# Kernel optimization log

Measured on AMD Instinct MI355X. Metric: run time of the kernel, lower is better.

Reference implementation:

```python
import jax, jax.numpy as jnp
import numpy as np

N = 100000          # num nodes
E = 500000          # num edges
D_IN = 32           # in_channels
D_OUT = 32          # out_channels (== in_channels, required by per-edge bmm)
NUM_REL = 16


def setup_inputs() -> dict:
    key = jax.random.key(0)
    k1, k2, k3, k4, k5, k6 = jax.random.split(key, 6)
    x = jax.random.normal(k1, (N, D_IN), dtype=jnp.float32)
    edge_index = jax.random.randint(k2, (2, E), 0, N)
    edge_type = jax.random.randint(k3, (E,), 0, NUM_REL)
    # Linear(in, out, bias=False): weight stored [in, out] here (x @ W)
    W = jax.random.normal(k4, (D_IN, D_OUT), dtype=jnp.float32) / np.sqrt(D_IN)
    # nn.Embedding(num_relations, in*out)
    rel_emb = jax.random.normal(k5, (NUM_REL, D_IN * D_OUT), dtype=jnp.float32)
    # attention vector, xavier-uniform-ish
    lim = float(1.414 * np.sqrt(6.0 / (D_OUT + 1)))
    attention = jax.random.uniform(k6, (D_OUT, 1), minval=-lim, maxval=lim, dtype=jnp.float32)
    return {"x": x, "edge_index": edge_index, "edge_type": edge_type,
            "W": W, "rel_emb": rel_emb, "attention": attention}


def reference(x, edge_index, edge_type, W, rel_emb, attention):
    # x = self.weight(x)
    h = x @ W                                            # [N, D_OUT]
    # per-edge relation transform: rel_trans [E, D_IN, D_OUT]
    rel = rel_emb[edge_type].reshape(-1, D_IN, D_OUT)    # [E, D_IN, D_OUT]
    src = edge_index[0]
    dst = edge_index[1]
    # messages = bmm(x[src], rel_trans) -> per-edge matvec
    msg = jnp.einsum('ei,eio->eo', h[src], rel)          # [E, D_OUT]
    # scatter-add into destination node buckets
    out = jax.ops.segment_sum(msg, dst, num_segments=N)  # [N, D_OUT]
    # global attention softmax over all nodes (dim=0)
    scores = (out @ attention)[:, 0]                     # [N]
    weights = jax.nn.softmax(scores, axis=0)             # [N]
    # dropout omitted (eval mode / deterministic reference)
    out = jax.nn.relu(out * weights[:, None])
    return out
```

## Files before the change

kernel.cpp:

```cpp
#include <hip/hip_runtime.h>

static constexpr int NN  = 100000;
static constexpr int NE  = 500000;
static constexpr int D   = 32;
static constexpr int NR  = 16;
static constexpr int HB  = 256;
static constexpr int ES  = (NE + HB - 1) / HB;
static constexpr int CAP = 33000;
static constexpr int NY  = 128;

__global__ __launch_bounds__(256) void k_prep(const int* __restrict__ ei,
                                              const int* __restrict__ et,
                                              const float* __restrict__ W,
                                              const float* __restrict__ rel,
                                              float* __restrict__ wr,
                                              int* __restrict__ cursor,
                                              int2* __restrict__ rec,
                                              float* __restrict__ outz) {
    __shared__ int lh[NR], lcur[NR];
    if (threadIdx.x < NR) lh[threadIdx.x] = 0;
    __syncthreads();

    {
        float4* oz = reinterpret_cast<float4*>(outz);
        const int total4 = NN * D / 4;
        for (int i = blockIdx.x * 256 + threadIdx.x; i < total4; i += HB * 256)
            oz[i] = make_float4(0.f, 0.f, 0.f, 0.f);
    }

    if (blockIdx.x < NR) {
        const int t = blockIdx.x;
        for (int idx = threadIdx.x; idx < D * D; idx += 256) {
            const int i = idx >> 5;
            const int o = idx & 31;
            const float* Wr = W + i * D;
            const float* Rr = rel + t * (D * D) + o;
            float s = 0.f;
            #pragma unroll
            for (int j = 0; j < D; ++j)
                s = fmaf(Wr[j], Rr[j * D], s);
            wr[t * (D * D) + idx] = s;
        }
    }

    const int beg = blockIdx.x * ES, end = min(beg + ES, NE);
    for (int e = beg + (int)threadIdx.x; e < end; e += 256)
        atomicAdd(&lh[et[e]], 1);
    __syncthreads();
    if (threadIdx.x < NR)
        lcur[threadIdx.x] = (lh[threadIdx.x] > 0)
                          ? atomicAdd(&cursor[threadIdx.x], lh[threadIdx.x])
                          : 0;
    __syncthreads();
    for (int e = beg + (int)threadIdx.x; e < end; e += 256) {
        const int t = et[e];
        const int rank = min(atomicAdd(&lcur[t], 1), CAP - 1);
        rec[t * CAP + rank] = make_int2(ei[e], ei[NE + e]);
    }
}

__global__ __launch_bounds__(256) void k_edge(const float* __restrict__ x,
                                              const int2* __restrict__ rec,
                                              const int* __restrict__ cnt,
                                              const float* __restrict__ wr,
                                              float* __restrict__ acc) {
    const int t    = blockIdx.x & (NR - 1);
    const int c    = blockIdx.x >> 4;
    const int lane = threadIdx.x & 63;
    const int wv   = threadIdx.x >> 6;
    const int half = lane >> 5;
    const int o    = lane & 31;
    const int r8   = lane >> 3;
    const int q8   = lane & 7;

    __shared__ float sx[4][2][8][36];
    __shared__ int   sd[4][2][8];

    float Rc[32];
    {
        const float* __restrict__ Rt = wr + t * 1024;
        #pragma unroll
        for (int i = 0; i < 32; ++i) Rc[i] = Rt[i * 32 + o];
    }

    const int beg  = t * CAP;
    const int cntt = min(cnt[t], CAP);
    if (cntt <= 0) return;
    const int elast = beg + cntt - 1;
    const int ngrp  = (cntt + 7) >> 3;
    const int nw    = NY * 4;
    const int wid   = c * 4 + wv;
    if (wid >= ngrp) return;

    int2 rr0 = rec[min(beg + wid * 8 + r8, elast)];
    int2 rr1 = rec[min(beg + (wid + nw) * 8 + r8, elast)];
    int2 rr2 = rec[min(beg + (wid + 2 * nw) * 8 + r8, elast)];
    float4 xv0 = reinterpret_cast<const float4*>(x + (size_t)rr0.x * D)[q8];

    int buf = 0;
    for (int grp = wid; grp < ngrp; grp += nw) {
        *reinterpret_cast<float4*>(&sx[wv][buf][r8][q8 * 4]) = xv0;
        if (q8 == 0) sd[wv][buf][r8] = rr0.y;

        float4 xv1 = reinterpret_cast<const float4*>(x + (size_t)rr1.x * D)[q8];
        int2 rr3 = rec[min(beg + (grp + 3 * nw) * 8 + r8, elast)];

        __asm__ volatile("s_waitcnt lgkmcnt(0)" ::: "memory");

        const int lbase = grp * 8;
        #pragma unroll
        for (int jj = 0; jj < 4; ++jj) {
            const int row = jj * 2 + half;
            const float* rp = &sx[wv][buf][row][0];
            float p = 0.f;
            #pragma unroll
            for (int q = 0; q < 8; ++q) {
                const float4 v = *reinterpret_cast<const float4*>(rp + q * 4);
                p = fmaf(v.x, Rc[4*q+0], p);
                p = fmaf(v.y, Rc[4*q+1], p);
                p = fmaf(v.z, Rc[4*q+2], p);
                p = fmaf(v.w, Rc[4*q+3], p);
            }
            if (lbase + row < cntt) {
                const int dd = sd[wv][buf][row];
                atomicAdd(acc + (size_t)dd * D + o, p);
            }
        }
        rr0 = rr1; rr1 = rr2; rr2 = rr3; xv0 = xv1;
        buf ^= 1;
    }
}

__global__ __launch_bounds__(256) void k_score(const float* __restrict__ acc,
                                               const float* __restrict__ att,
                                               float* __restrict__ scores,
                                               float* __restrict__ pmax,
                                               float* __restrict__ psum) {
    __shared__ float sA[D];
    __shared__ float shm[4], shs[4];
    if (threadIdx.x < D) sA[threadIdx.x] = att[threadIdx.x];
    __syncthreads();
    const int n = blockIdx.x * 256 + threadIdx.x;
    float s = -3.4e38f;
    if (n < NN) {
        const float4* av = reinterpret_cast<const float4*>(acc + (size_t)n * D);
        float v0 = 0.f;
        #pragma unroll
        for (int k = 0; k < 8; ++k) {
            float4 v = av[k];
            v0 += v.x * sA[4*k+0] + v.y * sA[4*k+1] + v.z * sA[4*k+2] + v.w * sA[4*k+3];
        }
        scores[n] = v0;
        s = v0;
    }
    float m = s;
    #pragma unroll
    for (int offt = 32; offt > 0; offt >>= 1)
        m = fmaxf(m, __shfl_down(m, offt, 64));
    if ((threadIdx.x & 63) == 0) shm[threadIdx.x >> 6] = m;
    __syncthreads();
    const float bm = fmaxf(fmaxf(shm[0], shm[1]), fmaxf(shm[2], shm[3]));
    float e = (n < NN) ? expf(s - bm) : 0.f;
    #pragma unroll
    for (int offt = 32; offt > 0; offt >>= 1)
        e += __shfl_down(e, offt, 64);
    if ((threadIdx.x & 63) == 0) shs[threadIdx.x >> 6] = e;
    __syncthreads();
    if (threadIdx.x == 0) {
        pmax[blockIdx.x] = bm;
        psum[blockIdx.x] = shs[0] + shs[1] + shs[2] + shs[3];
    }
}

__global__ __launch_bounds__(256) void k_final(float* __restrict__ out,
                                               const float* __restrict__ scores,
                                               const float* __restrict__ pmax,
                                               const float* __restrict__ psum,
                                               int nb) {
    __shared__ float shm[4], shs[4];
    const int tid = threadIdx.x;
    float m = -3.4e38f, s = 0.f;
    for (int i = tid; i < nb; i += 256) {
        const float mi = pmax[i], si = psum[i];
        const float M = fmaxf(m, mi);
        s = s * expf(m - M) + si * expf(mi - M);
        m = M;
    }
    #pragma unroll
    for (int offt = 32; offt > 0; offt >>= 1) {
        const float mo = __shfl_down(m, offt, 64);
        const float so = __shfl_down(s, offt, 64);
        const float M = fmaxf(m, mo);
        s = s * expf(m - M) + so * expf(mo - M);
        m = M;
    }
    if ((tid & 63) == 0) { shm[tid >> 6] = m; shs[tid >> 6] = s; }
    __syncthreads();
    float M = shm[0], S = shs[0];
    #pragma unroll
    for (int w = 1; w < 4; ++w) {
        const float Mn = fmaxf(M, shm[w]);
        S = S * expf(M - Mn) + shs[w] * expf(shm[w] - Mn);
        M = Mn;
    }
    const int idx = blockIdx.x * 256 + tid;
    const int n = idx >> 3;
    const float w = expf(scores[n] - M) / S;
    float4* p = reinterpret_cast<float4*>(out);
    float4 v = p[idx];
    v.x = fmaxf(v.x * w, 0.f);
    v.y = fmaxf(v.y * w, 0.f);
    v.z = fmaxf(v.z * w, 0.f);
    v.w = fmaxf(v.w * w, 0.f);
    p[idx] = v;
}

extern "C" void kernel_launch(void* const* d_in, const int* in_sizes, int n_in,
                              void* d_out, int out_size, void* d_ws, size_t ws_size,
                              hipStream_t stream) {
    const float* x   = (const float*)d_in[0];
    const int*   ei  = (const int*)  d_in[1];
    const int*   et  = (const int*)  d_in[2];
    const float* W   = (const float*)d_in[3];
    const float* rel = (const float*)d_in[4];
    const float* att = (const float*)d_in[5];
    float* out = (float*)d_out;

    float* wr     = (float*)d_ws;
    int2*  rec    = (int2*)(wr + NR * D * D);
    int*   cursor = (int*)(rec + NR * CAP);
    float* pmax   = (float*)(cursor + NR);
    float* psum   = pmax + 512;
    float* scores = (float*)rec;

    hipMemsetAsync(cursor, 0, NR * sizeof(int), stream);

    k_prep<<<HB, 256, 0, stream>>>(ei, et, W, rel, wr, cursor, rec, out);
    k_edge<<<NR * NY, 256, 0, stream>>>(x, rec, cursor, wr, out);

    const int nb_n = (NN + 255) / 256;
    k_score<<<nb_n, 256, 0, stream>>>(out, att, scores, pmax, psum);
    k_final<<<(NN * (D / 4)) / 256, 256, 0, stream>>>(out, scores, pmax, psum, nb_n);
}
```

Before: 95.89 us.

## Accumulate messages in fp16 half2 atomics and fuse attention score into edge kernel

Switches the scatter-add accumulator from fp32 to fp16 using packed half2 atomics, halving the number and size of atomic ops per edge. It also computes the attention score per edge with a cross-lane shuffle reduction and accumulates it with one fp32 atomic per edge. This removes the score kernel's full read of the accumulator. The final kernel converts fp16 back to fp32 output. This risks accuracy loss from fp16 accumulation and adds shuffle work in the edge loop.

Result: faster. 88.47 us, median of 2 (-7.7%).

```diff
diff --git a/kernel.cpp b/kernel.cpp
--- a/kernel.cpp
+++ b/kernel.cpp
@@ -1,4 +1,5 @@
 #include <hip/hip_runtime.h>
+#include <hip/hip_fp16.h>
 
 static constexpr int NN  = 100000;
 static constexpr int NE  = 500000;
@@ -16,16 +17,15 @@
                                               float* __restrict__ wr,
                                               int* __restrict__ cursor,
                                               int2* __restrict__ rec,
-                                              float* __restrict__ outz) {
+                                              float4* __restrict__ zbase) {
     __shared__ int lh[NR], lcur[NR];
     if (threadIdx.x < NR) lh[threadIdx.x] = 0;
     __syncthreads();
 
     {
-        float4* oz = reinterpret_cast<float4*>(outz);
-        const int total4 = NN * D / 4;
+        const int total4 = (NN * D * 2 + NN * 4) / 16;
         for (int i = blockIdx.x * 256 + threadIdx.x; i < total4; i += HB * 256)
-            oz[i] = make_float4(0.f, 0.f, 0.f, 0.f);
+            zbase[i] = make_float4(0.f, 0.f, 0.f, 0.f);
     }
 
     if (blockIdx.x < NR) {
@@ -63,7 +63,9 @@
                                               const int2* __restrict__ rec,
                                               const int* __restrict__ cnt,
                                               const float* __restrict__ wr,
-                                              float* __restrict__ acc) {
+                                              const float* __restrict__ att,
+                                              __half* __restrict__ acc16,
+                                              float* __restrict__ scores) {
     const int t    = blockIdx.x & (NR - 1);
     const int c    = blockIdx.x >> 4;
     const int lane = threadIdx.x & 63;
@@ -76,6 +78,7 @@
     __shared__ float sx[4][2][8][36];
     __shared__ int   sd[4][2][8];
 
+    const float atto = att[o];
     float Rc[32];
     {
         const float* __restrict__ Rt = wr + t * 1024;
@@ -123,7 +126,19 @@
             }
             if (lbase + row < cntt) {
                 const int dd = sd[wv][buf][row];
-                atomicAdd(acc + (size_t)dd * D + o, p);
+                float v = p * atto;
+                v += __shfl_xor(v, 1, 64);
+                v += __shfl_xor(v, 2, 64);
+                v += __shfl_xor(v, 4, 64);
+                v += __shfl_xor(v, 8, 64);
+                v += __shfl_xor(v, 16, 64);
+                if (o == 0) atomicAdd(scores + dd, v);
+                const float pp = __shfl_xor(p, 1, 64);
+                if ((o & 1) == 0) {
+                    __half2 hv = __halves2half2(__float2half(p), __float2half(pp));
+                    unsafeAtomicAdd(reinterpret_cast<__half2*>(
+                        acc16 + (size_t)dd * D + o), hv);
+                }
             }
         }
         rr0 = rr1; rr1 = rr2; rr2 = rr3; xv0 = xv1;
@@ -131,28 +146,12 @@
     }
 }
 
-__global__ __launch_bounds__(256) void k_score(const float* __restrict__ acc,
-                                               const float* __restrict__ att,
-                                               float* __restrict__ scores,
+__global__ __launch_bounds__(256) void k_score(const float* __restrict__ scores,
                                                float* __restrict__ pmax,
                                                float* __restrict__ psum) {
-    __shared__ float sA[D];
     __shared__ float shm[4], shs[4];
-    if (threadIdx.x < D) sA[threadIdx.x] = att[threadIdx.x];
-    __syncthreads();
     const int n = blockIdx.x * 256 + threadIdx.x;
-    float s = -3.4e38f;
-    if (n < NN) {
-        const float4* av = reinterpret_cast<const float4*>(acc + (size_t)n * D);
-        float v0 = 0.f;
-        #pragma unroll
-        for (int k = 0; k < 8; ++k) {
-            float4 v = av[k];
-            v0 += v.x * sA[4*k+0] + v.y * sA[4*k+1] + v.z * sA[4*k+2] + v.w * sA[4*k+3];
-        }
-        scores[n] = v0;
-        s = v0;
-    }
+    const float s = (n < NN) ? scores[n] : -3.4e38f;
     float m = s;
     #pragma unroll
     for (int offt = 32; offt > 0; offt >>= 1)
@@ -172,10 +171,11 @@
     }
 }
 
-__global__ __launch_bounds__(256) void k_final(float* __restrict__ out,
+__global__ __launch_bounds__(256) void k_final(const __half* __restrict__ acc16,
                                                const float* __restrict__ scores,
                                                const float* __restrict__ pmax,
                                                const float* __restrict__ psum,
+                                               float* __restrict__ out,
                                                int nb) {
     __shared__ float shm[4], shs[4];
     const int tid = threadIdx.x;
@@ -204,15 +204,25 @@
         M = Mn;
     }
     const int idx = blockIdx.x * 256 + tid;
-    const int n = idx >> 3;
+    if (idx >= NN * 4) return;
+    const int n  = idx >> 2;
+    const int co = (idx & 3) * 8;
     const float w = expf(scores[n] - M) / S;
-    float4* p = reinterpret_cast<float4*>(out);
-    float4 v = p[idx];
-    v.x = fmaxf(v.x * w, 0.f);
-    v.y = fmaxf(v.y * w, 0.f);
-    v.z = fmaxf(v.z * w, 0.f);
-    v.w = fmaxf(v.w * w, 0.f);
-    p[idx] = v;
+    const __half2* hp = reinterpret_cast<const __half2*>(acc16 + (size_t)n * D + co);
+    float4 o0, o1;
+    {
+        float2 f0 = __half22float2(hp[0]);
+        float2 f1 = __half22float2(hp[1]);
+        float2 f2 = __half22float2(hp[2]);
+        float2 f3 = __half22float2(hp[3]);
+        o0.x = fmaxf(f0.x * w, 0.f); o0.y = fmaxf(f0.y * w, 0.f);
+        o0.z = fmaxf(f1.x * w, 0.f); o0.w = fmaxf(f1.y * w, 0.f);
+        o1.x = fmaxf(f2.x * w, 0.f); o1.y = fmaxf(f2.y * w, 0.f);
+        o1.z = fmaxf(f3.x * w, 0.f); o1.w = fmaxf(f3.y * w, 0.f);
+    }
+    float4* op = reinterpret_cast<float4*>(out + (size_t)n * D + co);
+    op[0] = o0;
+    op[1] = o1;
 }
 
 extern "C" void kernel_launch(void* const* d_in, const int* in_sizes, int n_in,
@@ -226,19 +236,22 @@
     const float* att = (const float*)d_in[5];
     float* out = (float*)d_out;
 
-    float* wr     = (float*)d_ws;
-    int2*  rec    = (int2*)(wr + NR * D * D);
-    int*   cursor = (int*)(rec + NR * CAP);
-    float* pmax   = (float*)(cursor + NR);
-    float* psum   = pmax + 512;
-    float* scores = (float*)rec;
+    float*  wr     = (float*)d_ws;
+    __half* acc16  = (__half*)(wr + NR * D * D);
+    float*  scores = (float*)(acc16 + (size_t)NN * D);
+    int2*   rec    = (int2*)(scores + NN);
+    int*    cursor = (int*)(rec + NR * CAP);
+    float*  pmax   = (float*)(cursor + NR);
+    float*  psum   = pmax + 512;
 
     hipMemsetAsync(cursor, 0, NR * sizeof(int), stream);
 
-    k_prep<<<HB, 256, 0, stream>>>(ei, et, W, rel, wr, cursor, rec, out);
-    k_edge<<<NR * NY, 256, 0, stream>>>(x, rec, cursor, wr, out);
+    k_prep<<<HB, 256, 0, stream>>>(ei, et, W, rel, wr, cursor, rec,
+                                   (float4*)acc16);
+    k_edge<<<NR * NY, 256, 0, stream>>>(x, rec, cursor, wr, att, acc16, scores);
 
     const int nb_n = (NN + 255) / 256;
-    k_score<<<nb_n, 256, 0, stream>>>(out, att, scores, pmax, psum);
-    k_final<<<(NN * (D / 4)) / 256, 256, 0, stream>>>(out, scores, pmax, psum, nb_n);
-}
+    k_score<<<nb_n, 256, 0, stream>>>(scores, pmax, psum);
+    k_final<<<(NN * 4 + 255) / 256, 256, 0, stream>>>(acc16, scores, pmax, psum,
+                                                      out, nb_n);
+}
```
